# Performance work log

Measured on AMD Instinct MI355X. Metric: run time of the kernel, lower is better.

Reference implementation:

```python
import jax, jax.numpy as jnp
import numpy as np

NUM_EMBEDDINGS = 1024
EMBEDDING_DIM = 64


def setup_inputs() -> dict:
    key = jax.random.key(0)
    k1, k2 = jax.random.split(key)
    z = jax.random.normal(k1, (64, 32, 32, EMBEDDING_DIM), dtype=jnp.float32)
    # torch init: uniform_(-1/num_embeddings, 1/num_embeddings)
    lim = 1.0 / NUM_EMBEDDINGS
    codebook = jax.random.uniform(
        k2, (NUM_EMBEDDINGS, EMBEDDING_DIM), dtype=jnp.float32,
        minval=-lim, maxval=lim)
    return {"z": z, "codebook": codebook}


def reference(z, codebook):
    # z: [..., D]; codebook: [K, D]
    z_flat = z.reshape(-1, z.shape[-1])                      # [N, D]
    # ||z||^2 - 2 z.e + ||e||^2  -> [N, K]
    distances = (
        jnp.sum(z_flat ** 2, axis=1, keepdims=True)
        - 2.0 * jnp.einsum("nd,kd->nk", z_flat, codebook)
        + jnp.sum(codebook ** 2, axis=1)
    )
    min_indices = jnp.argmin(distances, axis=1)              # [N]
    z_q = jnp.take(codebook, min_indices, axis=0).reshape(z.shape)
    return z_q, min_indices
```

## Files before the change

### kernel.cpp

```cpp
#include <hip/hip_runtime.h>
#include <hip/hip_bf16.h>
#include <math.h>


#define D      64
#define K      1024
#define BR     128
#define CT     64
#define NCT    (K / CT)
#define STR32  68
#define STR16  72
#define BLOCK  256

typedef _Float16 half8_t __attribute__((ext_vector_type(8)));
typedef _Float16 half4_t __attribute__((ext_vector_type(4)));
typedef float    floatx4 __attribute__((ext_vector_type(4)));

__device__ __forceinline__ float np_sumsq64_p(const float* __restrict__ x) {
    float r[8];
    {
        float4 v0 = *(const float4*)(x);
        float4 v1 = *(const float4*)(x + 4);
        r[0] = __fmul_rn(v0.x, v0.x); r[1] = __fmul_rn(v0.y, v0.y);
        r[2] = __fmul_rn(v0.z, v0.z); r[3] = __fmul_rn(v0.w, v0.w);
        r[4] = __fmul_rn(v1.x, v1.x); r[5] = __fmul_rn(v1.y, v1.y);
        r[6] = __fmul_rn(v1.z, v1.z); r[7] = __fmul_rn(v1.w, v1.w);
    }
#pragma unroll
    for (int i = 8; i < 64; i += 8) {
        float4 v0 = *(const float4*)(x + i);
        float4 v1 = *(const float4*)(x + i + 4);
        r[0] = __fadd_rn(r[0], __fmul_rn(v0.x, v0.x));
        r[1] = __fadd_rn(r[1], __fmul_rn(v0.y, v0.y));
        r[2] = __fadd_rn(r[2], __fmul_rn(v0.z, v0.z));
        r[3] = __fadd_rn(r[3], __fmul_rn(v0.w, v0.w));
        r[4] = __fadd_rn(r[4], __fmul_rn(v1.x, v1.x));
        r[5] = __fadd_rn(r[5], __fmul_rn(v1.y, v1.y));
        r[6] = __fadd_rn(r[6], __fmul_rn(v1.z, v1.z));
        r[7] = __fadd_rn(r[7], __fmul_rn(v1.w, v1.w));
    }
    return __fadd_rn(__fadd_rn(__fadd_rn(r[0], r[1]), __fadd_rn(r[2], r[3])),
                     __fadd_rn(__fadd_rn(r[4], r[5]), __fadd_rn(r[6], r[7])));
}

__global__ __launch_bounds__(BLOCK, 2) void vq_mfma_kernel(
    const float* __restrict__ z, const float* __restrict__ cb,
    float* __restrict__ zq, float* __restrict__ idx_out) {
    __shared__ __align__(16) char smem[BR * STR32 * 4];
    float*    zf = (float*)smem;
    _Float16* e1 = (_Float16*)smem;
    _Float16* e2 = e1 + CT * STR16;
    __shared__ float sS[BR];
    __shared__ float sCn[CT];
    __shared__ int   sBi[BR];

    const int tid  = threadIdx.x;
    const int lane = tid & 63;
    const int wv   = tid >> 6;
    const int quad = lane >> 4;
    const int l16  = lane & 15;
    const long rowbase = (long)blockIdx.x * BR;

    const float4* gz = (const float4*)(z + rowbase * D);
#pragma unroll
    for (int i = 0; i < 8; ++i) {
        int idx4 = i * BLOCK + tid;
        int r = idx4 >> 4, j = idx4 & 15;
        float4 v = gz[idx4];
        *(float4*)(zf + r * STR32 + j * 4) = v;
    }
    __syncthreads();

    if (tid < BR) sS[tid] = np_sumsq64_p(zf + tid * STR32);

    half8_t a1[2][2], a2[2][2];
#pragma unroll
    for (int rt = 0; rt < 2; ++rt) {
        const int row = wv * 32 + rt * 16 + l16;
#pragma unroll
        for (int ch = 0; ch < 2; ++ch) {
            const float* p = zf + row * STR32 + ch * 32 + quad * 8;
            float4 f0 = *(const float4*)(p);
            float4 f1 = *(const float4*)(p + 4);
            float xs[8] = {f0.x, f0.y, f0.z, f0.w, f1.x, f1.y, f1.z, f1.w};
#pragma unroll
            for (int j = 0; j < 8; ++j) {
                _Float16 h1 = (_Float16)xs[j];
                a1[rt][ch][j] = h1;
                a2[rt][ch][j] =
                    (_Float16)(__fmul_rn(__fsub_rn(xs[j], (float)h1), 2048.0f));
            }
        }
    }

    float bv[2][4];
    int   bi[2][4];
#pragma unroll
    for (int rt = 0; rt < 2; ++rt)
#pragma unroll
        for (int r = 0; r < 4; ++r) { bv[rt][r] = INFINITY; bi[rt][r] = 0; }

    for (int tI = 0; tI < NCT; ++tI) {
        const int kb = tI * CT;
        __syncthreads();
        const float4* gcb = (const float4*)(cb + (long)kb * D);
#pragma unroll
        for (int i = 0; i < 4; ++i) {
            int idx4 = i * BLOCK + tid;
            int c = idx4 >> 4, j = idx4 & 15;
            float4 v = gcb[idx4];
            half4_t h1v, h2v;
            float xs[4] = {v.x, v.y, v.z, v.w};
#pragma unroll
            for (int q = 0; q < 4; ++q) {
                float x10 = __fmul_rn(xs[q], 1024.0f);
                _Float16 g1 = (_Float16)x10;
                h1v[q] = g1;
                h2v[q] = (_Float16)(__fmul_rn(__fsub_rn(x10, (float)g1), 2048.0f));
            }
            *(half4_t*)(e1 + c * STR16 + j * 4) = h1v;
            *(half4_t*)(e2 + c * STR16 + j * 4) = h2v;
        }
        if (tid < CT) sCn[tid] = np_sumsq64_p(cb + (long)(kb + tid) * D);
        __syncthreads();

        half8_t b1[4][2], b2[4][2];
#pragma unroll
        for (int ct = 0; ct < 4; ++ct) {
            const int c = ct * 16 + l16;
#pragma unroll
            for (int ch = 0; ch < 2; ++ch) {
                b1[ct][ch] = *(const half8_t*)(e1 + c * STR16 + ch * 32 + quad * 8);
                b2[ct][ch] = *(const half8_t*)(e2 + c * STR16 + ch * 32 + quad * 8);
            }
        }

#pragma unroll
        for (int rt = 0; rt < 2; ++rt) {
            floatx4 accM[4], accC[4];
#pragma unroll
            for (int ct = 0; ct < 4; ++ct) {
                accM[ct] = (floatx4){0.f, 0.f, 0.f, 0.f};
                accC[ct] = (floatx4){0.f, 0.f, 0.f, 0.f};
            }
#pragma unroll
            for (int ch = 0; ch < 2; ++ch)
#pragma unroll
                for (int ct = 0; ct < 4; ++ct) {
                    accM[ct] = __builtin_amdgcn_mfma_f32_16x16x32_f16(
                        a1[rt][ch], b1[ct][ch], accM[ct], 0, 0, 0);
                    accC[ct] = __builtin_amdgcn_mfma_f32_16x16x32_f16(
                        a1[rt][ch], b2[ct][ch], accC[ct], 0, 0, 0);
                    accC[ct] = __builtin_amdgcn_mfma_f32_16x16x32_f16(
                        a2[rt][ch], b1[ct][ch], accC[ct], 0, 0, 0);
                }
            float Sv[4];
#pragma unroll
            for (int r = 0; r < 4; ++r)
                Sv[r] = sS[wv * 32 + rt * 16 + quad * 4 + r];
#pragma unroll
            for (int ct = 0; ct < 4; ++ct) {
                const float cn = sCn[ct * 16 + l16];
                const int kg = kb + ct * 16 + l16;
#pragma unroll
                for (int r = 0; r < 4; ++r) {
                    float ds = fmaf(accC[ct][r], 0x1p-11f, accM[ct][r]);
                    float t2 = __fmul_rn(ds, 0x1p-9f);
                    float dist = __fadd_rn(__fsub_rn(Sv[r], t2), cn);
                    if (dist < bv[rt][r]) { bv[rt][r] = dist; bi[rt][r] = kg; }
                }
            }
        }
    }

#pragma unroll
    for (int rt = 0; rt < 2; ++rt) {
#pragma unroll
        for (int r = 0; r < 4; ++r) {
            float v = bv[rt][r];
            int   x = bi[rt][r];
#pragma unroll
            for (int off = 1; off <= 8; off <<= 1) {
                float ov = __shfl_xor(v, off);
                int   ox = __shfl_xor(x, off);
                if (ov < v || (ov == v && ox < x)) { v = ov; x = ox; }
            }
            if (l16 == 0) {
                const int rl = wv * 32 + rt * 16 + quad * 4 + r;
                sBi[rl] = x;
                idx_out[rowbase + rl] = (float)x;
            }
        }
    }
    __syncthreads();

    const float4* cb4 = (const float4*)cb;
    float4* zq4 = (float4*)(zq + rowbase * D);
#pragma unroll
    for (int i = 0; i < 8; ++i) {
        int idx4 = i * BLOCK + tid;
        int r = idx4 >> 4, j = idx4 & 15;
        zq4[idx4] = cb4[(long)sBi[r] * 16 + j];
    }
}

extern "C" void kernel_launch(void* const* d_in, const int* in_sizes, int n_in,
                              void* d_out, int out_size, void* d_ws, size_t ws_size,
                              hipStream_t stream) {
    const float* z  = (const float*)d_in[0];
    const float* cb = (const float*)d_in[1];

    const int n_rows = in_sizes[0] / D;
    float* zq      = (float*)d_out;
    float* idx_out = zq + (long)n_rows * D;

    const int grid = n_rows / BR;
    vq_mfma_kernel<<<grid, BLOCK, 0, stream>>>(z, cb, zq, idx_out);
}
```

Baseline: 116.2 us.

## Precompute fp16 codebook splits, split K across blocks, merge via atomicMin

A prepass kernel converts the codebook into a pre-swizzled hi/lo fp16 layout and computes codebook norms once, instead of every block redoing this conversion in LDS. The main kernel splits the 1024 codes into two halves per row block, doubling the grid and raising occupancy to 3 blocks per CU. It reads B fragments straight from global memory with no per-tile syncs, and merges per-row minima with a packed 64-bit atomicMin. A separate resolve kernel gathers the winning codebook rows. The cost is a memset plus three extra launches, and the packed key relies on distances being non-negative so float bits order correctly; negative distances could mis-order.

New measurement: 113.0 us. 2.8% less time.

```diff
diff --git a/kernel.cpp b/kernel.cpp
--- a/kernel.cpp
+++ b/kernel.cpp
@@ -6,15 +6,15 @@
 #define D      64
 #define K      1024
 #define BR     128
-#define CT     64
-#define NCT    (K / CT)
-#define STR32  68
-#define STR16  72
 #define BLOCK  256
 
 typedef _Float16 half8_t __attribute__((ext_vector_type(8)));
-typedef _Float16 half4_t __attribute__((ext_vector_type(4)));
 typedef float    floatx4 __attribute__((ext_vector_type(4)));
+typedef unsigned long long u64;
+
+#define WS_KEYS_OFF  0
+#define WS_CN_OFF    524288
+#define WS_EF_OFF    528384
 
 __device__ __forceinline__ float np_sumsq64_p(const float* __restrict__ x) {
     float r[8];
@@ -43,35 +43,59 @@
                      __fadd_rn(__fadd_rn(r[4], r[5]), __fadd_rn(r[6], r[7])));
 }
 
-__global__ __launch_bounds__(BLOCK, 2) void vq_mfma_kernel(
-    const float* __restrict__ z, const float* __restrict__ cb,
-    float* __restrict__ zq, float* __restrict__ idx_out) {
-    __shared__ __align__(16) char smem[BR * STR32 * 4];
-    float*    zf = (float*)smem;
-    _Float16* e1 = (_Float16*)smem;
-    _Float16* e2 = e1 + CT * STR16;
+__global__ void vq_pre(const float* __restrict__ cb, float* __restrict__ cn,
+                       _Float16* __restrict__ ef) {
+    const int k = blockIdx.x * 64 + threadIdx.x;
+    if (k >= K) return;
+    cn[k] = np_sumsq64_p(cb + (long)k * D);
+    const int t = k >> 6, ct = (k >> 4) & 3, l16 = k & 15;
+#pragma unroll
+    for (int ch = 0; ch < 2; ++ch)
+#pragma unroll
+        for (int quad = 0; quad < 4; ++quad) {
+            const float* p = cb + (long)k * D + ch * 32 + quad * 8;
+            half8_t h1, h2;
+#pragma unroll
+            for (int j = 0; j < 8; ++j) {
+                float x10 = __fmul_rn(p[j], 1024.0f);
+                _Float16 g1 = (_Float16)x10;
+                h1[j] = g1;
+                h2[j] = (_Float16)(__fmul_rn(__fsub_rn(x10, (float)g1), 2048.0f));
+            }
+            const int base = t * 8192 + 128 * quad + 8 * l16;
+            *(half8_t*)(ef + base + 512 * (ch * 4 + ct))       = h1;
+            *(half8_t*)(ef + base + 512 * ((2 + ch) * 4 + ct)) = h2;
+        }
+}
+
+__global__ __launch_bounds__(BLOCK, 3) void vq_main(
+    const float* __restrict__ z, const _Float16* __restrict__ ef,
+    const float* __restrict__ cn, u64* __restrict__ keys) {
+    __shared__ __align__(16) float zf[BR * 68];
     __shared__ float sS[BR];
-    __shared__ float sCn[CT];
-    __shared__ int   sBi[BR];
+    __shared__ float sCn[512];
 
     const int tid  = threadIdx.x;
     const int lane = tid & 63;
     const int wv   = tid >> 6;
     const int quad = lane >> 4;
     const int l16  = lane & 15;
-    const long rowbase = (long)blockIdx.x * BR;
+    const int rb = blockIdx.x >> 1, ks = blockIdx.x & 1;
+    const long rowbase = (long)rb * BR;
+    const int kb0 = ks * 512;
 
     const float4* gz = (const float4*)(z + rowbase * D);
 #pragma unroll
     for (int i = 0; i < 8; ++i) {
         int idx4 = i * BLOCK + tid;
         int r = idx4 >> 4, j = idx4 & 15;
-        float4 v = gz[idx4];
-        *(float4*)(zf + r * STR32 + j * 4) = v;
-    }
+        *(float4*)(zf + r * 68 + j * 4) = gz[idx4];
+    }
+    sCn[tid]       = cn[kb0 + tid];
+    sCn[tid + 256] = cn[kb0 + tid + 256];
     __syncthreads();
 
-    if (tid < BR) sS[tid] = np_sumsq64_p(zf + tid * STR32);
+    if (tid < BR) sS[tid] = np_sumsq64_p(zf + tid * 68);
 
     half8_t a1[2][2], a2[2][2];
 #pragma unroll
@@ -79,7 +103,7 @@
         const int row = wv * 32 + rt * 16 + l16;
 #pragma unroll
         for (int ch = 0; ch < 2; ++ch) {
-            const float* p = zf + row * STR32 + ch * 32 + quad * 8;
+            const float* p = zf + row * 68 + ch * 32 + quad * 8;
             float4 f0 = *(const float4*)(p);
             float4 f1 = *(const float4*)(p + 4);
             float xs[8] = {f0.x, f0.y, f0.z, f0.w, f1.x, f1.y, f1.z, f1.w};
@@ -92,6 +116,14 @@
             }
         }
     }
+    __syncthreads();
+
+    float myS[2][4];
+#pragma unroll
+    for (int rt = 0; rt < 2; ++rt)
+#pragma unroll
+        for (int r = 0; r < 4; ++r)
+            myS[rt][r] = sS[wv * 32 + rt * 16 + quad * 4 + r];
 
     float bv[2][4];
     int   bi[2][4];
@@ -100,81 +132,61 @@
 #pragma unroll
         for (int r = 0; r < 4; ++r) { bv[rt][r] = INFINITY; bi[rt][r] = 0; }
 
-    for (int tI = 0; tI < NCT; ++tI) {
-        const int kb = tI * CT;
-        __syncthreads();
-        const float4* gcb = (const float4*)(cb + (long)kb * D);
-#pragma unroll
-        for (int i = 0; i < 4; ++i) {
-            int idx4 = i * BLOCK + tid;
-            int c = idx4 >> 4, j = idx4 & 15;
-            float4 v = gcb[idx4];
-            half4_t h1v, h2v;
-            float xs[4] = {v.x, v.y, v.z, v.w};
-#pragma unroll
-            for (int q = 0; q < 4; ++q) {
-                float x10 = __fmul_rn(xs[q], 1024.0f);
-                _Float16 g1 = (_Float16)x10;
-                h1v[q] = g1;
-                h2v[q] = (_Float16)(__fmul_rn(__fsub_rn(x10, (float)g1), 2048.0f));
-            }
-            *(half4_t*)(e1 + c * STR16 + j * 4) = h1v;
-            *(half4_t*)(e2 + c * STR16 + j * 4) = h2v;
-        }
-        if (tid < CT) sCn[tid] = np_sumsq64_p(cb + (long)(kb + tid) * D);
-        __syncthreads();
-
-        half8_t b1[4][2], b2[4][2];
-#pragma unroll
-        for (int ct = 0; ct < 4; ++ct) {
-            const int c = ct * 16 + l16;
-#pragma unroll
-            for (int ch = 0; ch < 2; ++ch) {
-                b1[ct][ch] = *(const half8_t*)(e1 + c * STR16 + ch * 32 + quad * 8);
-                b2[ct][ch] = *(const half8_t*)(e2 + c * STR16 + ch * 32 + quad * 8);
-            }
-        }
-
-#pragma unroll
-        for (int rt = 0; rt < 2; ++rt) {
-            floatx4 accM[4], accC[4];
-#pragma unroll
-            for (int ct = 0; ct < 4; ++ct) {
-                accM[ct] = (floatx4){0.f, 0.f, 0.f, 0.f};
-                accC[ct] = (floatx4){0.f, 0.f, 0.f, 0.f};
-            }
-#pragma unroll
-            for (int ch = 0; ch < 2; ++ch)
-#pragma unroll
-                for (int ct = 0; ct < 4; ++ct) {
-                    accM[ct] = __builtin_amdgcn_mfma_f32_16x16x32_f16(
-                        a1[rt][ch], b1[ct][ch], accM[ct], 0, 0, 0);
-                    accC[ct] = __builtin_amdgcn_mfma_f32_16x16x32_f16(
-                        a1[rt][ch], b2[ct][ch], accC[ct], 0, 0, 0);
-                    accC[ct] = __builtin_amdgcn_mfma_f32_16x16x32_f16(
-                        a2[rt][ch], b1[ct][ch], accC[ct], 0, 0, 0);
+    const _Float16* eb = ef + (long)ks * 8 * 8192;
+
+    for (int t = 0; t < 8; ++t) {
+        const _Float16* tb = eb + t * 8192 + 8 * lane;
+        const int kbase = kb0 + t * 64;
+#pragma unroll
+        for (int ctp = 0; ctp < 2; ++ctp) {
+            half8_t b1[2][2], b2[2][2];
+#pragma unroll
+            for (int ct2 = 0; ct2 < 2; ++ct2) {
+                const int ct = ctp * 2 + ct2;
+#pragma unroll
+                for (int ch = 0; ch < 2; ++ch) {
+                    b1[ct2][ch] = *(const half8_t*)(tb + 512 * (ch * 4 + ct));
+                    b2[ct2][ch] = *(const half8_t*)(tb + 512 * ((2 + ch) * 4 + ct));
                 }
-            float Sv[4];
-#pragma unroll
-            for (int r = 0; r < 4; ++r)
-                Sv[r] = sS[wv * 32 + rt * 16 + quad * 4 + r];
-#pragma unroll
-            for (int ct = 0; ct < 4; ++ct) {
-                const float cn = sCn[ct * 16 + l16];
-                const int kg = kb + ct * 16 + l16;
-#pragma unroll
-                for (int r = 0; r < 4; ++r) {
-                    float ds = fmaf(accC[ct][r], 0x1p-11f, accM[ct][r]);
-                    float t2 = __fmul_rn(ds, 0x1p-9f);
-                    float dist = __fadd_rn(__fsub_rn(Sv[r], t2), cn);
-                    if (dist < bv[rt][r]) { bv[rt][r] = dist; bi[rt][r] = kg; }
+            }
+#pragma unroll
+            for (int rt = 0; rt < 2; ++rt) {
+                floatx4 aM[2], aC[2];
+#pragma unroll
+                for (int c = 0; c < 2; ++c) {
+                    aM[c] = (floatx4){0.f, 0.f, 0.f, 0.f};
+                    aC[c] = (floatx4){0.f, 0.f, 0.f, 0.f};
                 }
-            }
-        }
-    }
-
-#pragma unroll
-    for (int rt = 0; rt < 2; ++rt) {
+#pragma unroll
+                for (int ch = 0; ch < 2; ++ch)
+#pragma unroll
+                    for (int c = 0; c < 2; ++c) {
+                        aM[c] = __builtin_amdgcn_mfma_f32_16x16x32_f16(
+                            a1[rt][ch], b1[c][ch], aM[c], 0, 0, 0);
+                        aC[c] = __builtin_amdgcn_mfma_f32_16x16x32_f16(
+                            a1[rt][ch], b2[c][ch], aC[c], 0, 0, 0);
+                        aC[c] = __builtin_amdgcn_mfma_f32_16x16x32_f16(
+                            a2[rt][ch], b1[c][ch], aC[c], 0, 0, 0);
+                    }
+#pragma unroll
+                for (int c = 0; c < 2; ++c) {
+                    const int ct = ctp * 2 + c;
+                    const float cnv = sCn[t * 64 + ct * 16 + l16];
+                    const int kg = kbase + ct * 16 + l16;
+#pragma unroll
+                    for (int r = 0; r < 4; ++r) {
+                        float ds = fmaf(aC[c][r], 0x1p-11f, aM[c][r]);
+                        float t2 = __fmul_rn(ds, 0x1p-9f);
+                        float dist = __fadd_rn(__fsub_rn(myS[rt][r], t2), cnv);
+                        if (dist < bv[rt][r]) { bv[rt][r] = dist; bi[rt][r] = kg; }
+                    }
+                }
+            }
+        }
+    }
+
+#pragma unroll
+    for (int rt = 0; rt < 2; ++rt)
 #pragma unroll
         for (int r = 0; r < 4; ++r) {
             float v = bv[rt][r];
@@ -186,22 +198,21 @@
                 if (ov < v || (ov == v && ox < x)) { v = ov; x = ox; }
             }
             if (l16 == 0) {
-                const int rl = wv * 32 + rt * 16 + quad * 4 + r;
-                sBi[rl] = x;
-                idx_out[rowbase + rl] = (float)x;
-            }
-        }
-    }
-    __syncthreads();
-
-    const float4* cb4 = (const float4*)cb;
-    float4* zq4 = (float4*)(zq + rowbase * D);
-#pragma unroll
-    for (int i = 0; i < 8; ++i) {
-        int idx4 = i * BLOCK + tid;
-        int r = idx4 >> 4, j = idx4 & 15;
-        zq4[idx4] = cb4[(long)sBi[r] * 16 + j];
-    }
+                const long row = rowbase + wv * 32 + rt * 16 + quad * 4 + r;
+                u64 key = ((u64)__float_as_uint(v) << 32) | (unsigned)x;
+                atomicMin(&keys[row], key);
+            }
+        }
+}
+
+__global__ void vq_resolve(const float* __restrict__ cb,
+                           const u64* __restrict__ keys,
+                           float* __restrict__ zq, float* __restrict__ idx_out) {
+    const int gid = blockIdx.x * BLOCK + threadIdx.x;
+    const int row = gid >> 4, j = gid & 15;
+    const unsigned k = (unsigned)(keys[row] & 0xFFFFFFFFu);
+    ((float4*)zq)[gid] = ((const float4*)cb)[(long)k * 16 + j];
+    if (j == 0) idx_out[row] = (float)k;
 }
 
 extern "C" void kernel_launch(void* const* d_in, const int* in_sizes, int n_in,
@@ -214,6 +225,12 @@
     float* zq      = (float*)d_out;
     float* idx_out = zq + (long)n_rows * D;
 
-    const int grid = n_rows / BR;
-    vq_mfma_kernel<<<grid, BLOCK, 0, stream>>>(z, cb, zq, idx_out);
-}
+    u64*      ws_keys = (u64*)((char*)d_ws + WS_KEYS_OFF);
+    float*    ws_cn   = (float*)((char*)d_ws + WS_CN_OFF);
+    _Float16* ws_ef   = (_Float16*)((char*)d_ws + WS_EF_OFF);
+
+    hipMemsetAsync(ws_keys, 0xFF, (size_t)n_rows * sizeof(u64), stream);
+    vq_pre<<<K / 64, 64, 0, stream>>>(cb, ws_cn, ws_ef);
+    vq_main<<<(n_rows / BR) * 2, BLOCK, 0, stream>>>(z, ws_ef, ws_cn, ws_keys);
+    vq_resolve<<<(n_rows * 16) / BLOCK, BLOCK, 0, stream>>>(cb, ws_keys, zq, idx_out);
+}
```
